# Performance work log

Hardware: AMD Instinct MI355X
Metric: run time of the kernel (lower is better)

The kernel has to match this reference:

```python
import jax, jax.numpy as jnp
import numpy as np

N = 50000      # nodes
E = 1600000    # edges (avg degree 32)
DIN, DH, DOUT = 256, 128, 64


def gcn_conv(x, W, b, row, col, w, n):
    """One GCNConv layer (self-loops already appended to row/col/w).
    row = source nodes, col = target nodes; aggregate at targets."""
    xw = x @ W                                        # [n, d_out]
    deg = jax.ops.segment_sum(w, col, num_segments=n)  # in-degree weighted
    dinv = jnp.where(deg > 0, jax.lax.rsqrt(deg), 0.0)
    norm = dinv[row] * w * dinv[col]                  # [E+n]
    msg = norm[:, None] * xw[row]                     # [E+n, d_out] gather
    out = jax.ops.segment_sum(msg, col, num_segments=n)
    return out + b


def setup_inputs() -> dict:
    key = jax.random.key(0)
    k = jax.random.split(key, 6)
    x = jax.random.normal(k[0], (N, DIN), dtype=jnp.float32)
    edge_index = jax.random.randint(k[1], (2, E), 0, N)
    edge_weight = jax.random.uniform(k[2], (E,), dtype=jnp.float32)
    W1 = jax.random.normal(k[3], (DIN, DH), dtype=jnp.float32) * (1.0 / np.sqrt(DIN))
    b1 = jnp.zeros((DH,), dtype=jnp.float32)
    W2 = jax.random.normal(k[4], (DH, DOUT), dtype=jnp.float32) * (1.0 / np.sqrt(DH))
    b2 = jnp.zeros((DOUT,), dtype=jnp.float32)
    return {"x": x, "edge_index": edge_index, "edge_weight": edge_weight,
            "W1": W1, "b1": b1, "W2": W2, "b2": b2}


def reference(x, edge_index, edge_weight, W1, b1, W2, b2):
    n = x.shape[0]
    loops = jnp.arange(n, dtype=edge_index.dtype)
    row = jnp.concatenate([edge_index[0], loops])
    col = jnp.concatenate([edge_index[1], loops])
    w = jnp.concatenate([edge_weight, jnp.ones((n,), dtype=edge_weight.dtype)])
    h = gcn_conv(x, W1, b1, row, col, w, n)
    h = jax.nn.relu(h)
    # dropout(p=0.2) is identity in eval mode
    h = gcn_conv(h, W2, b2, row, col, w, n)
    return jax.nn.log_softmax(h, axis=-1)
```

## Files before the change

### kernel.cpp

```cpp
#include <hip/hip_runtime.h>
#include <hip/hip_bf16.h>
#include <cstddef>


#define DIN 256
#define DH  128
#define DOUT 64
#define NPB 100
#define NBMAX 512

typedef __bf16 bf16x8 __attribute__((ext_vector_type(8)));
typedef float f32x4 __attribute__((ext_vector_type(4)));

__device__ __forceinline__ float bflo(unsigned u) { return __uint_as_float(u << 16); }
__device__ __forceinline__ float bfhi(unsigned u) { return __uint_as_float(u & 0xffff0000u); }
__device__ __forceinline__ unsigned short f2bf(float f) {
    unsigned u = __float_as_uint(f);
    unsigned r = (u + 0x7fffu + ((u >> 16) & 1u)) >> 16;
    return (unsigned short)r;
}

__global__ void prep_w_kernel(const float* __restrict__ W1, const float* __restrict__ W2,
                              unsigned short* __restrict__ wt1, unsigned short* __restrict__ wt2) {
    int i = blockIdx.x * 256 + threadIdx.x;
    if (i < DH * DIN) {
        int nn = i >> 8, k = i & 255;
        wt1[i] = f2bf(W1[k * DH + nn]);
    } else {
        int j = i - DH * DIN;
        if (j < DOUT * DH) {
            int nn = j >> 7, k = j & 127;
            wt2[j] = f2bf(W2[k * DOUT + nn]);
        }
    }
}

__launch_bounds__(256)
__global__ void hist_kernel(const int* __restrict__ col, int* __restrict__ bh,
                            int E, int Ec, int NB) {
    __shared__ int hist[NBMAX];
    int p = blockIdx.x, t = threadIdx.x;
    for (int b = t; b < NB; b += 256) hist[b] = 0;
    __syncthreads();
    int s = p * Ec, e = min(s + Ec, E);
    for (int i = s + t; i < e; i += 256) atomicAdd(&hist[col[i] / NPB], 1);
    __syncthreads();
    for (int b = t; b < NB; b += 256) bh[p * NB + b] = hist[b];
}

__launch_bounds__(512)
__global__ void colscan_kernel(int* __restrict__ bh, int* __restrict__ btotal,
                               int P, int NB) {
    __shared__ int arr[512];
    int b = blockIdx.x, t = threadIdx.x;
    arr[t] = (t < P) ? bh[t * NB + b] : 0;
    __syncthreads();
    for (int off = 1; off < 512; off <<= 1) {
        int v = (t >= off) ? arr[t - off] : 0;
        __syncthreads();
        arr[t] += v;
        __syncthreads();
    }
    int excl = (t == 0) ? 0 : arr[t - 1];
    if (t < P) bh[t * NB + b] = excl;
    if (t == P - 1) btotal[b] = arr[t];
}

__launch_bounds__(512)
__global__ void basescan_kernel(const int* __restrict__ btotal, int* __restrict__ bbase,
                                int* __restrict__ rowptr, int NB, int n, int E) {
    __shared__ int arr[512];
    int t = threadIdx.x;
    arr[t] = (t < NB) ? btotal[t] : 0;
    __syncthreads();
    for (int off = 1; off < 512; off <<= 1) {
        int v = (t >= off) ? arr[t - off] : 0;
        __syncthreads();
        arr[t] += v;
        __syncthreads();
    }
    int excl = (t == 0) ? 0 : arr[t - 1];
    if (t <= NB) bbase[t] = excl;
    if (t == 511) rowptr[n] = E;
}

__launch_bounds__(256)
__global__ void scatter_kernel(const int* __restrict__ row, const int* __restrict__ col,
                               const float* __restrict__ w, const int* __restrict__ bh,
                               const int* __restrict__ bbase, int2* __restrict__ part,
                               int E, int Ec, int NB) {
    __shared__ int cur[NBMAX];
    int p = blockIdx.x, t = threadIdx.x;
    for (int b = t; b < NB; b += 256) cur[b] = bbase[b] + bh[p * NB + b];
    __syncthreads();
    int s = p * Ec, e = min(s + Ec, E);
    for (int i = s + t; i < e; i += 256) {
        int c = col[i];
        int r = row[i];
        int b = c / NPB;
        int pos = atomicAdd(&cur[b], 1);
        part[pos] = make_int2(r | ((c - b * NPB) << 16), __float_as_int(w[i]));
    }
}

__launch_bounds__(256)
__global__ void bucket_csr_kernel(const int2* __restrict__ part, const int* __restrict__ bbase,
                                  float* __restrict__ dinv, int* __restrict__ rowptr,
                                  int2* __restrict__ final_e, int n) {
    __shared__ int   hist[NPB];
    __shared__ float wsum[NPB];
    __shared__ int   nbase[NPB];
    __shared__ int   cur[NPB];
    int b = blockIdx.x, t = threadIdx.x;
    if (t < NPB) { hist[t] = 0; wsum[t] = 0.0f; }
    __syncthreads();
    int s = bbase[b], e = bbase[b + 1];
    for (int i = s + t; i < e; i += 256) {
        int2 rec = part[i];
        int cl = rec.x >> 16;
        atomicAdd(&hist[cl], 1);
        atomicAdd(&wsum[cl], __int_as_float(rec.y));
    }
    __syncthreads();
    if (t == 0) {
        int run = 0;
        for (int k = 0; k < NPB; ++k) { nbase[k] = run; run += hist[k]; }
    }
    __syncthreads();
    if (t < NPB) {
        int node = b * NPB + t;
        if (node < n) {
            dinv[node] = rsqrtf(1.0f + wsum[t]);
            rowptr[node] = s + nbase[t];
        }
        cur[t] = nbase[t];
    }
    __syncthreads();
    for (int i = s + t; i < e; i += 256) {
        int2 rec = part[i];
        int cl = rec.x >> 16;
        int q = s + atomicAdd(&cur[cl], 1);
        final_e[q] = make_int2(rec.x & 0xffff, rec.y);
    }
}

template <int K, int M>
__launch_bounds__(256)
__global__ void gemm_mfma_kernel(const float* __restrict__ A,
                                 const unsigned short* __restrict__ Wt,
                                 const float* __restrict__ scale,
                                 unsigned short* __restrict__ C, int N) {
    constexpr int BK = 64, LD = BK + 8;
    constexpr int WN = M / 4;
    constexpr int NT = WN / 16;
    constexpr int CLD = M + 8;
    constexpr int SM = (64 * LD + M * LD) > (64 * CLD) ? (64 * LD + M * LD) : (64 * CLD);
    __shared__ unsigned short smem[SM];
    __shared__ float sdv[64];
    unsigned short* As = smem;
    unsigned short* Bs = smem + 64 * LD;

    const int tid = threadIdx.x;
    const int row0 = blockIdx.x * 64;
    const int lane = tid & 63;
    const int quad = lane >> 4, r16 = lane & 15;
    const int n0 = (tid >> 6) * WN;

    if (tid < 64) {
        int r = row0 + tid;
        sdv[tid] = (r < N) ? scale[r] : 0.0f;
    }

    f32x4 acc[4][NT];
#pragma unroll
    for (int mt = 0; mt < 4; ++mt)
#pragma unroll
        for (int nt = 0; nt < NT; ++nt)
            acc[mt][nt] = (f32x4){0.f, 0.f, 0.f, 0.f};

    for (int k0 = 0; k0 < K; k0 += BK) {
#pragma unroll
        for (int j = 0; j < 4; ++j) {
            int idx = tid + j * 256;
            int m = idx >> 4;
            int q = idx & 15;
            int gr = row0 + m;
            float4 v = make_float4(0.f, 0.f, 0.f, 0.f);
            if (gr < N) v = *(const float4*)&A[(size_t)gr * K + k0 + q * 4];
            ushort4 s4;
            s4.x = f2bf(v.x); s4.y = f2bf(v.y); s4.z = f2bf(v.z); s4.w = f2bf(v.w);
            *(ushort4*)&As[m * LD + q * 4] = s4;
        }
#pragma unroll
        for (int j = 0; j < M * 8 / 256; ++j) {
            int idx = tid + j * 256;
            int nn = idx >> 3;
            int q = idx & 7;
            uint4 v = *(const uint4*)&Wt[(size_t)nn * K + k0 + q * 8];
            *(uint4*)&Bs[nn * LD + q * 8] = v;
        }
        __syncthreads();
#pragma unroll
        for (int ks = 0; ks < BK / 32; ++ks) {
            bf16x8 af[4], bfr[NT];
#pragma unroll
            for (int nt = 0; nt < NT; ++nt)
                bfr[nt] = *(const bf16x8*)&Bs[(n0 + nt * 16 + r16) * LD + ks * 32 + quad * 8];
#pragma unroll
            for (int mt = 0; mt < 4; ++mt)
                af[mt] = *(const bf16x8*)&As[(mt * 16 + r16) * LD + ks * 32 + quad * 8];
#pragma unroll
            for (int mt = 0; mt < 4; ++mt)
#pragma unroll
                for (int nt = 0; nt < NT; ++nt)
                    acc[mt][nt] = __builtin_amdgcn_mfma_f32_16x16x32_bf16(
                        af[mt], bfr[nt], acc[mt][nt], 0, 0, 0);
        }
        __syncthreads();
    }
    unsigned short* Cs = smem;
#pragma unroll
    for (int mt = 0; mt < 4; ++mt) {
#pragma unroll
        for (int i = 0; i < 4; ++i) {
            int r = mt * 16 + quad * 4 + i;
            float sc = sdv[r];
#pragma unroll
            for (int nt = 0; nt < NT; ++nt)
                Cs[r * CLD + n0 + nt * 16 + r16] = f2bf(acc[mt][nt][i] * sc);
        }
    }
    __syncthreads();
#pragma unroll
    for (int j = 0; j < 64 * M / 8 / 256; ++j) {
        int idx = tid + j * 256;
        int r = idx / (M / 8);
        int q = idx % (M / 8);
        int gr = row0 + r;
        if (gr < N) {
            uint4 v = *(const uint4*)&Cs[r * CLD + q * 8];
            *(uint4*)&C[(size_t)gr * M + q * 8] = v;
        }
    }
}

__launch_bounds__(256)
__global__ void agg1_kernel(const uint2* __restrict__ xw,
                            const int* __restrict__ rowptr,
                            const int2* __restrict__ edge,
                            const float* __restrict__ dinv,
                            const float* __restrict__ bias,
                            float* __restrict__ out, int n) {
    int node = blockIdx.x * 4 + (threadIdx.x >> 6);
    if (node >= n) return;
    int lane = threadIdx.x & 63;
    int half = lane >> 5, sub = lane & 31;
    float a0 = 0.f, a1 = 0.f, a2 = 0.f, a3 = 0.f;
    if (half == 0) {
        uint2 u = xw[(size_t)node * 32 + sub];
        a0 = bflo(u.x); a1 = bfhi(u.x); a2 = bflo(u.y); a3 = bfhi(u.y);
    }
    int p = rowptr[node], p1 = rowptr[node + 1];
    for (; p + 8 <= p1; p += 8) {
        int2 e0 = edge[p + half],     e1 = edge[p + 2 + half];
        int2 e2 = edge[p + 4 + half], e3 = edge[p + 6 + half];
        uint2 v0 = xw[(size_t)e0.x * 32 + sub];
        uint2 v1 = xw[(size_t)e1.x * 32 + sub];
        uint2 v2 = xw[(size_t)e2.x * 32 + sub];
        uint2 v3 = xw[(size_t)e3.x * 32 + sub];
        float w0 = __int_as_float(e0.y), w1 = __int_as_float(e1.y);
        float w2 = __int_as_float(e2.y), w3 = __int_as_float(e3.y);
        a0 += w0 * bflo(v0.x) + w1 * bflo(v1.x) + w2 * bflo(v2.x) + w3 * bflo(v3.x);
        a1 += w0 * bfhi(v0.x) + w1 * bfhi(v1.x) + w2 * bfhi(v2.x) + w3 * bfhi(v3.x);
        a2 += w0 * bflo(v0.y) + w1 * bflo(v1.y) + w2 * bflo(v2.y) + w3 * bflo(v3.y);
        a3 += w0 * bfhi(v0.y) + w1 * bfhi(v1.y) + w2 * bfhi(v2.y) + w3 * bfhi(v3.y);
    }
    for (; p + 2 <= p1; p += 2) {
        int2 e0 = edge[p + half];
        uint2 v0 = xw[(size_t)e0.x * 32 + sub];
        float w0 = __int_as_float(e0.y);
        a0 += w0 * bflo(v0.x); a1 += w0 * bfhi(v0.x);
        a2 += w0 * bflo(v0.y); a3 += w0 * bfhi(v0.y);
    }
    if (p < p1 && half == 0) {
        int2 e0 = edge[p];
        uint2 v0 = xw[(size_t)e0.x * 32 + sub];
        float w0 = __int_as_float(e0.y);
        a0 += w0 * bflo(v0.x); a1 += w0 * bfhi(v0.x);
        a2 += w0 * bflo(v0.y); a3 += w0 * bfhi(v0.y);
    }
    a0 += __shfl_xor(a0, 32); a1 += __shfl_xor(a1, 32);
    a2 += __shfl_xor(a2, 32); a3 += __shfl_xor(a3, 32);
    float di = dinv[node];
    float4 b = ((const float4*)bias)[sub];
    a0 = fmaxf(di * a0 + b.x, 0.f);
    a1 = fmaxf(di * a1 + b.y, 0.f);
    a2 = fmaxf(di * a2 + b.z, 0.f);
    a3 = fmaxf(di * a3 + b.w, 0.f);
    if (half == 0)
        ((float4*)out)[(size_t)node * 32 + sub] = make_float4(a0, a1, a2, a3);
}

__launch_bounds__(256)
__global__ void agg2_kernel(const uint2* __restrict__ xw,
                            const int* __restrict__ rowptr,
                            const int2* __restrict__ edge,
                            const float* __restrict__ dinv,
                            const float* __restrict__ bias,
                            float* __restrict__ out, int n) {
    int node = blockIdx.x * 4 + (threadIdx.x >> 6);
    if (node >= n) return;
    int lane = threadIdx.x & 63;
    int qw = lane >> 4, sub = lane & 15;
    float a0 = 0.f, a1 = 0.f, a2 = 0.f, a3 = 0.f;
    if (qw == 0) {
        uint2 u = xw[(size_t)node * 16 + sub];
        a0 = bflo(u.x); a1 = bfhi(u.x); a2 = bflo(u.y); a3 = bfhi(u.y);
    }
    int p = rowptr[node], p1 = rowptr[node + 1];
    for (; p + 8 <= p1; p += 8) {
        int2 e0 = edge[p + qw], e1 = edge[p + 4 + qw];
        uint2 v0 = xw[(size_t)e0.x * 16 + sub];
        uint2 v1 = xw[(size_t)e1.x * 16 + sub];
        float w0 = __int_as_float(e0.y), w1 = __int_as_float(e1.y);
        a0 += w0 * bflo(v0.x) + w1 * bflo(v1.x);
        a1 += w0 * bfhi(v0.x) + w1 * bfhi(v1.x);
        a2 += w0 * bflo(v0.y) + w1 * bflo(v1.y);
        a3 += w0 * bfhi(v0.y) + w1 * bfhi(v1.y);
    }
    for (; p + 4 <= p1; p += 4) {
        int2 e0 = edge[p + qw];
        uint2 v0 = xw[(size_t)e0.x * 16 + sub];
        float w0 = __int_as_float(e0.y);
        a0 += w0 * bflo(v0.x); a1 += w0 * bfhi(v0.x);
        a2 += w0 * bflo(v0.y); a3 += w0 * bfhi(v0.y);
    }
    int rem = p1 - p;
    if (qw < rem) {
        int2 e0 = edge[p + qw];
        uint2 v0 = xw[(size_t)e0.x * 16 + sub];
        float w0 = __int_as_float(e0.y);
        a0 += w0 * bflo(v0.x); a1 += w0 * bfhi(v0.x);
        a2 += w0 * bflo(v0.y); a3 += w0 * bfhi(v0.y);
    }
    a0 += __shfl_xor(a0, 32); a1 += __shfl_xor(a1, 32);
    a2 += __shfl_xor(a2, 32); a3 += __shfl_xor(a3, 32);
    a0 += __shfl_xor(a0, 16); a1 += __shfl_xor(a1, 16);
    a2 += __shfl_xor(a2, 16); a3 += __shfl_xor(a3, 16);
    float di = dinv[node];
    float4 b = ((const float4*)bias)[sub];
    a0 = di * a0 + b.x; a1 = di * a1 + b.y;
    a2 = di * a2 + b.z; a3 = di * a3 + b.w;
    float m = fmaxf(fmaxf(a0, a1), fmaxf(a2, a3));
#pragma unroll
    for (int off = 8; off > 0; off >>= 1) m = fmaxf(m, __shfl_xor(m, off));
    float s = __expf(a0 - m) + __expf(a1 - m) + __expf(a2 - m) + __expf(a3 - m);
#pragma unroll
    for (int off = 8; off > 0; off >>= 1) s += __shfl_xor(s, off);
    float lse = m + __logf(s);
    if (qw == 0)
        ((float4*)out)[(size_t)node * 16 + sub] =
            make_float4(a0 - lse, a1 - lse, a2 - lse, a3 - lse);
}

extern "C" void kernel_launch(void* const* d_in, const int* in_sizes, int n_in,
                              void* d_out, int out_size, void* d_ws, size_t ws_size,
                              hipStream_t stream) {
    const float* x  = (const float*)d_in[0];
    const int*   ei = (const int*)d_in[1];
    const float* ew = (const float*)d_in[2];
    const float* W1 = (const float*)d_in[3];
    const float* b1 = (const float*)d_in[4];
    const float* W2 = (const float*)d_in[5];
    const float* b2 = (const float*)d_in[6];
    float* out = (float*)d_out;

    const int n = in_sizes[0] / DIN;
    const int E = in_sizes[2];
    const int* row = ei;
    const int* col = ei + E;

    const int NB = (n + NPB - 1) / NPB;
    const int P  = NB;
    const int Ec = (E + P - 1) / P;

    char* ptr = (char*)d_ws;
    auto alloc = [&](size_t bytes) -> void* {
        void* r = (void*)ptr;
        ptr += (bytes + 255) & ~(size_t)255;
        return r;
    };
    int*   bh     = (int*)  alloc((size_t)P * NB * 4);
    int*   btotal = (int*)  alloc((size_t)NB * 4);
    int*   bbase  = (int*)  alloc((size_t)(NB + 1) * 4);
    int*   rowptr = (int*)  alloc((size_t)(n + 1) * 4);
    float* dinv   = (float*)alloc((size_t)n * 4);
    int2*  edge   = (int2*) alloc((size_t)E * 8);
    unsigned short* xw1 = (unsigned short*)alloc((size_t)n * DH * 2);
    unsigned short* wt1 = (unsigned short*)alloc((size_t)DH * DIN * 2);
    unsigned short* wt2 = (unsigned short*)alloc((size_t)DOUT * DH * 2);
    char* tail = (char*)alloc((size_t)n * DH * 4);
    int2*  part = (int2*)tail;
    float* h1   = (float*)tail;
    unsigned short* xw2 = xw1;

    const int nb_g = (n + 63) / 64;
    const int nb_a = (n + 3) / 4;

    prep_w_kernel<<<(DH * DIN + DOUT * DH + 255) / 256, 256, 0, stream>>>(W1, W2, wt1, wt2);
    hist_kernel<<<P, 256, 0, stream>>>(col, bh, E, Ec, NB);
    colscan_kernel<<<NB, 512, 0, stream>>>(bh, btotal, P, NB);
    basescan_kernel<<<1, 512, 0, stream>>>(btotal, bbase, rowptr, NB, n, E);
    scatter_kernel<<<P, 256, 0, stream>>>(row, col, ew, bh, bbase, part, E, Ec, NB);
    bucket_csr_kernel<<<NB, 256, 0, stream>>>(part, bbase, dinv, rowptr, edge, n);

    gemm_mfma_kernel<DIN, DH><<<nb_g, 256, 0, stream>>>(x, wt1, dinv, xw1, n);
    agg1_kernel<<<nb_a, 256, 0, stream>>>((const uint2*)xw1, rowptr, edge, dinv, b1, h1, n);
    gemm_mfma_kernel<DH, DOUT><<<nb_g, 256, 0, stream>>>(h1, wt2, dinv, xw2, n);
    agg2_kernel<<<nb_a, 256, 0, stream>>>((const uint2*)xw2, rowptr, edge, dinv, b2, out, n);
}
```

Measured before the change: 286.6 us.

## Slice feature tables into 32-column panels and aggregate each panel separately

The GEMM outputs are now stored as column-sliced panels of 32 features (64 bytes per node), and aggregation runs one pass per panel, with each wave handling 8 edges in parallel over 8 feature lanes. The aim is to shrink the gathered working set per pass so the randomly accessed table fits in cache and the per-edge gathers hit L2 more often. The second GEMM reads the sliced h1 layout directly, and log-softmax moves into a separate kernel. In exchange the edge list is read once per panel (six passes instead of two), more kernels are launched, and the logits make an extra round trip through memory.

```diff
diff --git a/kernel.cpp b/kernel.cpp
--- a/kernel.cpp
+++ b/kernel.cpp
@@ -144,7 +144,7 @@
     }
 }
 
-template <int K, int M>
+template <int K, int M, bool ASLICED>
 __launch_bounds__(256)
 __global__ void gemm_mfma_kernel(const float* __restrict__ A,
                                  const unsigned short* __restrict__ Wt,
@@ -185,8 +185,14 @@
             int m = idx >> 4;
             int q = idx & 15;
             int gr = row0 + m;
+            int k = k0 + q * 4;
             float4 v = make_float4(0.f, 0.f, 0.f, 0.f);
-            if (gr < N) v = *(const float4*)&A[(size_t)gr * K + k0 + q * 4];
+            if (gr < N) {
+                if (ASLICED)
+                    v = *(const float4*)&A[((size_t)(k >> 5) * N + gr) * 32 + (k & 31)];
+                else
+                    v = *(const float4*)&A[(size_t)gr * K + k];
+            }
             ushort4 s4;
             s4.x = f2bf(v.x); s4.y = f2bf(v.y); s4.z = f2bf(v.z); s4.w = f2bf(v.w);
             *(ushort4*)&As[m * LD + q * 4] = s4;
@@ -239,128 +245,76 @@
         int gr = row0 + r;
         if (gr < N) {
             uint4 v = *(const uint4*)&Cs[r * CLD + q * 8];
-            *(uint4*)&C[(size_t)gr * M + q * 8] = v;
-        }
-    }
-}
-
-__launch_bounds__(256)
-__global__ void agg1_kernel(const uint2* __restrict__ xw,
-                            const int* __restrict__ rowptr,
-                            const int2* __restrict__ edge,
-                            const float* __restrict__ dinv,
-                            const float* __restrict__ bias,
-                            float* __restrict__ out, int n) {
+            *(uint4*)&C[((size_t)(q >> 2) * N + gr) * 32 + (q & 3) * 8] = v;
+        }
+    }
+}
+
+template <bool RELU>
+__launch_bounds__(256)
+__global__ void agg_pass_kernel(const unsigned short* __restrict__ tbl,
+                                const int* __restrict__ rowptr,
+                                const int2* __restrict__ edge,
+                                const float* __restrict__ dinv,
+                                const float* __restrict__ bias,
+                                float* __restrict__ outs, int n) {
+    int node = blockIdx.x * 4 + (threadIdx.x >> 6);
+    if (node >= n) return;
+    const int lane = threadIdx.x & 63;
+    const int slot = lane >> 3;
+    const int fq = lane & 7;
+    const uint2* t = (const uint2*)tbl;
+
+    float a0 = 0.f, a1 = 0.f, a2 = 0.f, a3 = 0.f;
+    if (slot == 0) {
+        uint2 u = t[(size_t)node * 8 + fq];
+        a0 = bflo(u.x); a1 = bfhi(u.x); a2 = bflo(u.y); a3 = bfhi(u.y);
+    }
+    int p0 = rowptr[node], p1 = rowptr[node + 1];
+    for (int p = p0; p < p1; p += 16) {
+        int i0 = p + slot, i1 = p + 8 + slot;
+        bool v0 = i0 < p1, v1 = i1 < p1;
+        int2 e0 = edge[v0 ? i0 : p0];
+        int2 e1 = edge[v1 ? i1 : p0];
+        float w0 = v0 ? __int_as_float(e0.y) : 0.0f;
+        float w1 = v1 ? __int_as_float(e1.y) : 0.0f;
+        uint2 g0 = t[(size_t)e0.x * 8 + fq];
+        uint2 g1 = t[(size_t)e1.x * 8 + fq];
+        a0 += w0 * bflo(g0.x) + w1 * bflo(g1.x);
+        a1 += w0 * bfhi(g0.x) + w1 * bfhi(g1.x);
+        a2 += w0 * bflo(g0.y) + w1 * bflo(g1.y);
+        a3 += w0 * bfhi(g0.y) + w1 * bfhi(g1.y);
+    }
+#pragma unroll
+    for (int off = 8; off <= 32; off <<= 1) {
+        a0 += __shfl_xor(a0, off); a1 += __shfl_xor(a1, off);
+        a2 += __shfl_xor(a2, off); a3 += __shfl_xor(a3, off);
+    }
+    float di = dinv[node];
+    float4 b = ((const float4*)bias)[fq];
+    a0 = di * a0 + b.x; a1 = di * a1 + b.y;
+    a2 = di * a2 + b.z; a3 = di * a3 + b.w;
+    if (RELU) {
+        a0 = fmaxf(a0, 0.f); a1 = fmaxf(a1, 0.f);
+        a2 = fmaxf(a2, 0.f); a3 = fmaxf(a3, 0.f);
+    }
+    if (slot == 0)
+        ((float4*)outs)[(size_t)node * 8 + fq] = make_float4(a0, a1, a2, a3);
+}
+
+__launch_bounds__(256)
+__global__ void lsm_kernel(const float* __restrict__ lg, float* __restrict__ out, int n) {
     int node = blockIdx.x * 4 + (threadIdx.x >> 6);
     if (node >= n) return;
     int lane = threadIdx.x & 63;
-    int half = lane >> 5, sub = lane & 31;
-    float a0 = 0.f, a1 = 0.f, a2 = 0.f, a3 = 0.f;
-    if (half == 0) {
-        uint2 u = xw[(size_t)node * 32 + sub];
-        a0 = bflo(u.x); a1 = bfhi(u.x); a2 = bflo(u.y); a3 = bfhi(u.y);
-    }
-    int p = rowptr[node], p1 = rowptr[node + 1];
-    for (; p + 8 <= p1; p += 8) {
-        int2 e0 = edge[p + half],     e1 = edge[p + 2 + half];
-        int2 e2 = edge[p + 4 + half], e3 = edge[p + 6 + half];
-        uint2 v0 = xw[(size_t)e0.x * 32 + sub];
-        uint2 v1 = xw[(size_t)e1.x * 32 + sub];
-        uint2 v2 = xw[(size_t)e2.x * 32 + sub];
-        uint2 v3 = xw[(size_t)e3.x * 32 + sub];
-        float w0 = __int_as_float(e0.y), w1 = __int_as_float(e1.y);
-        float w2 = __int_as_float(e2.y), w3 = __int_as_float(e3.y);
-        a0 += w0 * bflo(v0.x) + w1 * bflo(v1.x) + w2 * bflo(v2.x) + w3 * bflo(v3.x);
-        a1 += w0 * bfhi(v0.x) + w1 * bfhi(v1.x) + w2 * bfhi(v2.x) + w3 * bfhi(v3.x);
-        a2 += w0 * bflo(v0.y) + w1 * bflo(v1.y) + w2 * bflo(v2.y) + w3 * bflo(v3.y);
-        a3 += w0 * bfhi(v0.y) + w1 * bfhi(v1.y) + w2 * bfhi(v2.y) + w3 * bfhi(v3.y);
-    }
-    for (; p + 2 <= p1; p += 2) {
-        int2 e0 = edge[p + half];
-        uint2 v0 = xw[(size_t)e0.x * 32 + sub];
-        float w0 = __int_as_float(e0.y);
-        a0 += w0 * bflo(v0.x); a1 += w0 * bfhi(v0.x);
-        a2 += w0 * bflo(v0.y); a3 += w0 * bfhi(v0.y);
-    }
-    if (p < p1 && half == 0) {
-        int2 e0 = edge[p];
-        uint2 v0 = xw[(size_t)e0.x * 32 + sub];
-        float w0 = __int_as_float(e0.y);
-        a0 += w0 * bflo(v0.x); a1 += w0 * bfhi(v0.x);
-        a2 += w0 * bflo(v0.y); a3 += w0 * bfhi(v0.y);
-    }
-    a0 += __shfl_xor(a0, 32); a1 += __shfl_xor(a1, 32);
-    a2 += __shfl_xor(a2, 32); a3 += __shfl_xor(a3, 32);
-    float di = dinv[node];
-    float4 b = ((const float4*)bias)[sub];
-    a0 = fmaxf(di * a0 + b.x, 0.f);
-    a1 = fmaxf(di * a1 + b.y, 0.f);
-    a2 = fmaxf(di * a2 + b.z, 0.f);
-    a3 = fmaxf(di * a3 + b.w, 0.f);
-    if (half == 0)
-        ((float4*)out)[(size_t)node * 32 + sub] = make_float4(a0, a1, a2, a3);
-}
-
-__launch_bounds__(256)
-__global__ void agg2_kernel(const uint2* __restrict__ xw,
-                            const int* __restrict__ rowptr,
-                            const int2* __restrict__ edge,
-                            const float* __restrict__ dinv,
-                            const float* __restrict__ bias,
-                            float* __restrict__ out, int n) {
-    int node = blockIdx.x * 4 + (threadIdx.x >> 6);
-    if (node >= n) return;
-    int lane = threadIdx.x & 63;
-    int qw = lane >> 4, sub = lane & 15;
-    float a0 = 0.f, a1 = 0.f, a2 = 0.f, a3 = 0.f;
-    if (qw == 0) {
-        uint2 u = xw[(size_t)node * 16 + sub];
-        a0 = bflo(u.x); a1 = bfhi(u.x); a2 = bflo(u.y); a3 = bfhi(u.y);
-    }
-    int p = rowptr[node], p1 = rowptr[node + 1];
-    for (; p + 8 <= p1; p += 8) {
-        int2 e0 = edge[p + qw], e1 = edge[p + 4 + qw];
-        uint2 v0 = xw[(size_t)e0.x * 16 + sub];
-        uint2 v1 = xw[(size_t)e1.x * 16 + sub];
-        float w0 = __int_as_float(e0.y), w1 = __int_as_float(e1.y);
-        a0 += w0 * bflo(v0.x) + w1 * bflo(v1.x);
-        a1 += w0 * bfhi(v0.x) + w1 * bfhi(v1.x);
-        a2 += w0 * bflo(v0.y) + w1 * bflo(v1.y);
-        a3 += w0 * bfhi(v0.y) + w1 * bfhi(v1.y);
-    }
-    for (; p + 4 <= p1; p += 4) {
-        int2 e0 = edge[p + qw];
-        uint2 v0 = xw[(size_t)e0.x * 16 + sub];
-        float w0 = __int_as_float(e0.y);
-        a0 += w0 * bflo(v0.x); a1 += w0 * bfhi(v0.x);
-        a2 += w0 * bflo(v0.y); a3 += w0 * bfhi(v0.y);
-    }
-    int rem = p1 - p;
-    if (qw < rem) {
-        int2 e0 = edge[p + qw];
-        uint2 v0 = xw[(size_t)e0.x * 16 + sub];
-        float w0 = __int_as_float(e0.y);
-        a0 += w0 * bflo(v0.x); a1 += w0 * bfhi(v0.x);
-        a2 += w0 * bflo(v0.y); a3 += w0 * bfhi(v0.y);
-    }
-    a0 += __shfl_xor(a0, 32); a1 += __shfl_xor(a1, 32);
-    a2 += __shfl_xor(a2, 32); a3 += __shfl_xor(a3, 32);
-    a0 += __shfl_xor(a0, 16); a1 += __shfl_xor(a1, 16);
-    a2 += __shfl_xor(a2, 16); a3 += __shfl_xor(a3, 16);
-    float di = dinv[node];
-    float4 b = ((const float4*)bias)[sub];
-    a0 = di * a0 + b.x; a1 = di * a1 + b.y;
-    a2 = di * a2 + b.z; a3 = di * a3 + b.w;
-    float m = fmaxf(fmaxf(a0, a1), fmaxf(a2, a3));
-#pragma unroll
-    for (int off = 8; off > 0; off >>= 1) m = fmaxf(m, __shfl_xor(m, off));
-    float s = __expf(a0 - m) + __expf(a1 - m) + __expf(a2 - m) + __expf(a3 - m);
-#pragma unroll
-    for (int off = 8; off > 0; off >>= 1) s += __shfl_xor(s, off);
-    float lse = m + __logf(s);
-    if (qw == 0)
-        ((float4*)out)[(size_t)node * 16 + sub] =
-            make_float4(a0 - lse, a1 - lse, a2 - lse, a3 - lse);
+    float v = lg[((size_t)(lane >> 5) * n + node) * 32 + (lane & 31)];
+    float m = v;
+#pragma unroll
+    for (int off = 32; off > 0; off >>= 1) m = fmaxf(m, __shfl_xor(m, off));
+    float s = __expf(v - m);
+#pragma unroll
+    for (int off = 32; off > 0; off >>= 1) s += __shfl_xor(s, off);
+    out[(size_t)node * 64 + lane] = v - m - __logf(s);
 }
 
 extern "C" void kernel_launch(void* const* d_in, const int* in_sizes, int n_in,
@@ -402,6 +356,7 @@
     char* tail = (char*)alloc((size_t)n * DH * 4);
     int2*  part = (int2*)tail;
     float* h1   = (float*)tail;
+    float* lg   = (float*)tail;
     unsigned short* xw2 = xw1;
 
     const int nb_g = (n + 63) / 64;
@@ -414,8 +369,15 @@
     scatter_kernel<<<P, 256, 0, stream>>>(row, col, ew, bh, bbase, part, E, Ec, NB);
     bucket_csr_kernel<<<NB, 256, 0, stream>>>(part, bbase, dinv, rowptr, edge, n);
 
-    gemm_mfma_kernel<DIN, DH><<<nb_g, 256, 0, stream>>>(x, wt1, dinv, xw1, n);
-    agg1_kernel<<<nb_a, 256, 0, stream>>>((const uint2*)xw1, rowptr, edge, dinv, b1, h1, n);
-    gemm_mfma_kernel<DH, DOUT><<<nb_g, 256, 0, stream>>>(h1, wt2, dinv, xw2, n);
-    agg2_kernel<<<nb_a, 256, 0, stream>>>((const uint2*)xw2, rowptr, edge, dinv, b2, out, n);
-}
+    gemm_mfma_kernel<DIN, DH, false><<<nb_g, 256, 0, stream>>>(x, wt1, dinv, xw1, n);
+    for (int s = 0; s < 4; ++s)
+        agg_pass_kernel<true><<<nb_a, 256, 0, stream>>>(
+            xw1 + (size_t)s * n * 32, rowptr, edge, dinv, b1 + 32 * s,
+            h1 + (size_t)s * n * 32, n);
+    gemm_mfma_kernel<DH, DOUT, true><<<nb_g, 256, 0, stream>>>(h1, wt2, dinv, xw2, n);
+    for (int s = 0; s < 2; ++s)
+        agg_pass_kernel<false><<<nb_a, 256, 0, stream>>>(
+            xw2 + (size_t)s * n * 32, rowptr, edge, dinv, b2 + 32 * s,
+            lg + (size_t)s * n * 32, n);
+    lsm_kernel<<<nb_a, 256, 0, stream>>>(lg, out, n);
+}
```

Measured after the change: 354.4 us. +23.6%, slower.

## Overlap edge scatter with first GEMM and fold source norm into edge weights

Applied to the files above, without the earlier changes.

The first GEMM no longer depends on dinv, because the source-side normalization is folded into the edge weights by a new normw pass. That lets the GEMM share one launch with the edge scatter, the two running as different block ranges. The partition count is reduced to a fixed 128 blocks, which shrinks the histogram and column-scan work. Nontemporal loads and stores are added for streaming edge and output traffic. The cost is an extra pass over the edge list, and the scatter blocks compete with the GEMM blocks for compute units.

```diff
diff --git a/kernel.cpp b/kernel.cpp
--- a/kernel.cpp
+++ b/kernel.cpp
@@ -8,9 +8,11 @@
 #define DOUT 64
 #define NPB 100
 #define NBMAX 512
+#define PBLK 128
 
 typedef __bf16 bf16x8 __attribute__((ext_vector_type(8)));
 typedef float f32x4 __attribute__((ext_vector_type(4)));
+typedef int i32x2 __attribute__((ext_vector_type(2)));
 
 __device__ __forceinline__ float bflo(unsigned u) { return __uint_as_float(u << 16); }
 __device__ __forceinline__ float bfhi(unsigned u) { return __uint_as_float(u & 0xffff0000u); }
@@ -18,6 +20,14 @@
     unsigned u = __float_as_uint(f);
     unsigned r = (u + 0x7fffu + ((u >> 16) & 1u)) >> 16;
     return (unsigned short)r;
+}
+__device__ __forceinline__ int2 ldnt2(const int2* p) {
+    i32x2 v = __builtin_nontemporal_load((const i32x2*)p);
+    int2 r; r.x = v.x; r.y = v.y; return r;
+}
+__device__ __forceinline__ void stnt4(float* p, float a, float b, float c, float d) {
+    f32x4 v = {a, b, c, d};
+    __builtin_nontemporal_store(v, (f32x4*)p);
 }
 
 __global__ void prep_w_kernel(const float* __restrict__ W1, const float* __restrict__ W2,
@@ -43,27 +53,27 @@
     for (int b = t; b < NB; b += 256) hist[b] = 0;
     __syncthreads();
     int s = p * Ec, e = min(s + Ec, E);
-    for (int i = s + t; i < e; i += 256) atomicAdd(&hist[col[i] / NPB], 1);
+    for (int i = s + t; i < e; i += 256)
+        atomicAdd(&hist[__builtin_nontemporal_load(&col[i]) / NPB], 1);
     __syncthreads();
     for (int b = t; b < NB; b += 256) bh[p * NB + b] = hist[b];
 }
 
-__launch_bounds__(512)
-__global__ void colscan_kernel(int* __restrict__ bh, int* __restrict__ btotal,
-                               int P, int NB) {
-    __shared__ int arr[512];
+__launch_bounds__(PBLK)
+__global__ void colscan_kernel(int* __restrict__ bh, int* __restrict__ btotal, int NB) {
+    __shared__ int arr[PBLK];
     int b = blockIdx.x, t = threadIdx.x;
-    arr[t] = (t < P) ? bh[t * NB + b] : 0;
-    __syncthreads();
-    for (int off = 1; off < 512; off <<= 1) {
-        int v = (t >= off) ? arr[t - off] : 0;
-        __syncthreads();
-        arr[t] += v;
-        __syncthreads();
-    }
-    int excl = (t == 0) ? 0 : arr[t - 1];
-    if (t < P) bh[t * NB + b] = excl;
-    if (t == P - 1) btotal[b] = arr[t];
+    int v = bh[t * NB + b];
+    arr[t] = v;
+    __syncthreads();
+    for (int off = 1; off < PBLK; off <<= 1) {
+        int u = (t >= off) ? arr[t - off] : 0;
+        __syncthreads();
+        arr[t] += u;
+        __syncthreads();
+    }
+    bh[t * NB + b] = arr[t] - v;
+    if (t == PBLK - 1) btotal[b] = arr[t];
 }
 
 __launch_bounds__(512)
@@ -84,98 +94,25 @@
     if (t == 511) rowptr[n] = E;
 }
 
-__launch_bounds__(256)
-__global__ void scatter_kernel(const int* __restrict__ row, const int* __restrict__ col,
-                               const float* __restrict__ w, const int* __restrict__ bh,
-                               const int* __restrict__ bbase, int2* __restrict__ part,
-                               int E, int Ec, int NB) {
-    __shared__ int cur[NBMAX];
-    int p = blockIdx.x, t = threadIdx.x;
-    for (int b = t; b < NB; b += 256) cur[b] = bbase[b] + bh[p * NB + b];
-    __syncthreads();
-    int s = p * Ec, e = min(s + Ec, E);
-    for (int i = s + t; i < e; i += 256) {
-        int c = col[i];
-        int r = row[i];
-        int b = c / NPB;
-        int pos = atomicAdd(&cur[b], 1);
-        part[pos] = make_int2(r | ((c - b * NPB) << 16), __float_as_int(w[i]));
-    }
-}
-
-__launch_bounds__(256)
-__global__ void bucket_csr_kernel(const int2* __restrict__ part, const int* __restrict__ bbase,
-                                  float* __restrict__ dinv, int* __restrict__ rowptr,
-                                  int2* __restrict__ final_e, int n) {
-    __shared__ int   hist[NPB];
-    __shared__ float wsum[NPB];
-    __shared__ int   nbase[NPB];
-    __shared__ int   cur[NPB];
-    int b = blockIdx.x, t = threadIdx.x;
-    if (t < NPB) { hist[t] = 0; wsum[t] = 0.0f; }
-    __syncthreads();
-    int s = bbase[b], e = bbase[b + 1];
-    for (int i = s + t; i < e; i += 256) {
-        int2 rec = part[i];
-        int cl = rec.x >> 16;
-        atomicAdd(&hist[cl], 1);
-        atomicAdd(&wsum[cl], __int_as_float(rec.y));
-    }
-    __syncthreads();
-    if (t == 0) {
-        int run = 0;
-        for (int k = 0; k < NPB; ++k) { nbase[k] = run; run += hist[k]; }
-    }
-    __syncthreads();
-    if (t < NPB) {
-        int node = b * NPB + t;
-        if (node < n) {
-            dinv[node] = rsqrtf(1.0f + wsum[t]);
-            rowptr[node] = s + nbase[t];
-        }
-        cur[t] = nbase[t];
-    }
-    __syncthreads();
-    for (int i = s + t; i < e; i += 256) {
-        int2 rec = part[i];
-        int cl = rec.x >> 16;
-        int q = s + atomicAdd(&cur[cl], 1);
-        final_e[q] = make_int2(rec.x & 0xffff, rec.y);
-    }
-}
-
 template <int K, int M>
-__launch_bounds__(256)
-__global__ void gemm_mfma_kernel(const float* __restrict__ A,
-                                 const unsigned short* __restrict__ Wt,
-                                 const float* __restrict__ scale,
-                                 unsigned short* __restrict__ C, int N) {
+__device__ __forceinline__ void gemm_body(const float* __restrict__ A,
+                                          const unsigned short* __restrict__ Wt,
+                                          unsigned short* __restrict__ C,
+                                          int N, int bid, int tid, char* sraw) {
     constexpr int BK = 64, LD = BK + 8;
-    constexpr int WN = M / 4;
-    constexpr int NT = WN / 16;
-    constexpr int CLD = M + 8;
-    constexpr int SM = (64 * LD + M * LD) > (64 * CLD) ? (64 * LD + M * LD) : (64 * CLD);
-    __shared__ unsigned short smem[SM];
-    __shared__ float sdv[64];
-    unsigned short* As = smem;
-    unsigned short* Bs = smem + 64 * LD;
-
-    const int tid = threadIdx.x;
-    const int row0 = blockIdx.x * 64;
+    constexpr int WN = M / 4, NTL = WN / 16, CLD = M + 8;
+    unsigned short* As = (unsigned short*)sraw;
+    unsigned short* Bs = As + 64 * LD;
+    const int row0 = bid * 64;
     const int lane = tid & 63;
     const int quad = lane >> 4, r16 = lane & 15;
     const int n0 = (tid >> 6) * WN;
 
-    if (tid < 64) {
-        int r = row0 + tid;
-        sdv[tid] = (r < N) ? scale[r] : 0.0f;
-    }
-
-    f32x4 acc[4][NT];
+    f32x4 acc[4][NTL];
 #pragma unroll
     for (int mt = 0; mt < 4; ++mt)
 #pragma unroll
-        for (int nt = 0; nt < NT; ++nt)
+        for (int nt = 0; nt < NTL; ++nt)
             acc[mt][nt] = (f32x4){0.f, 0.f, 0.f, 0.f};
 
     for (int k0 = 0; k0 < K; k0 += BK) {
@@ -202,9 +139,9 @@
         __syncthreads();
 #pragma unroll
         for (int ks = 0; ks < BK / 32; ++ks) {
-            bf16x8 af[4], bfr[NT];
-#pragma unroll
-            for (int nt = 0; nt < NT; ++nt)
+            bf16x8 af[4], bfr[NTL];
+#pragma unroll
+            for (int nt = 0; nt < NTL; ++nt)
                 bfr[nt] = *(const bf16x8*)&Bs[(n0 + nt * 16 + r16) * LD + ks * 32 + quad * 8];
 #pragma unroll
             for (int mt = 0; mt < 4; ++mt)
@@ -212,24 +149,22 @@
 #pragma unroll
             for (int mt = 0; mt < 4; ++mt)
 #pragma unroll
-                for (int nt = 0; nt < NT; ++nt)
+                for (int nt = 0; nt < NTL; ++nt)
                     acc[mt][nt] = __builtin_amdgcn_mfma_f32_16x16x32_bf16(
                         af[mt], bfr[nt], acc[mt][nt], 0, 0, 0);
         }
         __syncthreads();
     }
-    unsigned short* Cs = smem;
-#pragma unroll
-    for (int mt = 0; mt < 4; ++mt) {
+    unsigned short* Cs = (unsigned short*)sraw;
+#pragma unroll
+    for (int mt = 0; mt < 4; ++mt)
 #pragma unroll
         for (int i = 0; i < 4; ++i) {
             int r = mt * 16 + quad * 4 + i;
-            float sc = sdv[r];
-#pragma unroll
-            for (int nt = 0; nt < NT; ++nt)
-                Cs[r * CLD + n0 + nt * 16 + r16] = f2bf(acc[mt][nt][i] * sc);
-        }
-    }
+#pragma unroll
+            for (int nt = 0; nt < NTL; ++nt)
+                Cs[r * CLD + n0 + nt * 16 + r16] = f2bf(acc[mt][nt][i]);
+        }
     __syncthreads();
 #pragma unroll
     for (int j = 0; j < 64 * M / 8 / 256; ++j) {
@@ -241,6 +176,97 @@
             uint4 v = *(const uint4*)&Cs[r * CLD + q * 8];
             *(uint4*)&C[(size_t)gr * M + q * 8] = v;
         }
+    }
+}
+
+template <int K, int M>
+__launch_bounds__(256)
+__global__ void gemm_scatter_kernel(const float* __restrict__ A,
+                                    const unsigned short* __restrict__ Wt,
+                                    unsigned short* __restrict__ C, int N,
+                                    const int* __restrict__ row, const int* __restrict__ col,
+                                    const float* __restrict__ w, const int* __restrict__ bh,
+                                    const int* __restrict__ bbase, int2* __restrict__ part,
+                                    int E, int Ec, int NB) {
+    __shared__ char sraw[(64 + M) * (64 + 8) * 2];
+    int tid = threadIdx.x;
+    if ((int)blockIdx.x < PBLK) {
+        int* cur = (int*)sraw;
+        int p = blockIdx.x;
+        for (int b = tid; b < NB; b += 256) cur[b] = bbase[b] + bh[p * NB + b];
+        __syncthreads();
+        int s = p * Ec, e = min(s + Ec, E);
+        for (int i = s + tid; i < e; i += 256) {
+            int c = __builtin_nontemporal_load(&col[i]);
+            int r = __builtin_nontemporal_load(&row[i]);
+            float wv = __builtin_nontemporal_load(&w[i]);
+            int b = c / NPB;
+            int pos = atomicAdd(&cur[b], 1);
+            i32x2 rec; rec.x = r | ((c - b * NPB) << 16); rec.y = __float_as_int(wv);
+            __builtin_nontemporal_store(rec, (i32x2*)&part[pos]);
+        }
+    } else {
+        gemm_body<K, M>(A, Wt, C, N, blockIdx.x - PBLK, tid, sraw);
+    }
+}
+
+template <int K, int M>
+__launch_bounds__(256)
+__global__ void gemm_kernel(const float* __restrict__ A, const unsigned short* __restrict__ Wt,
+                            unsigned short* __restrict__ C, int N) {
+    __shared__ char sraw[(64 + M) * (64 + 8) * 2];
+    gemm_body<K, M>(A, Wt, C, N, blockIdx.x, threadIdx.x, sraw);
+}
+
+__launch_bounds__(256)
+__global__ void bucket_csr_kernel(const int2* __restrict__ part, const int* __restrict__ bbase,
+                                  float* __restrict__ dinv, int* __restrict__ rowptr,
+                                  int2* __restrict__ final_e, int n) {
+    __shared__ int   hist[NPB];
+    __shared__ float wsum[NPB];
+    __shared__ int   nbase[NPB];
+    __shared__ int   cur[NPB];
+    int b = blockIdx.x, t = threadIdx.x;
+    if (t < NPB) { hist[t] = 0; wsum[t] = 0.0f; }
+    __syncthreads();
+    int s = bbase[b], e = bbase[b + 1];
+    for (int i = s + t; i < e; i += 256) {
+        int2 rec = part[i];
+        int cl = rec.x >> 16;
+        atomicAdd(&hist[cl], 1);
+        atomicAdd(&wsum[cl], __int_as_float(rec.y));
+    }
+    __syncthreads();
+    if (t == 0) {
+        int run = 0;
+        for (int k = 0; k < NPB; ++k) { nbase[k] = run; run += hist[k]; }
+    }
+    __syncthreads();
+    if (t < NPB) {
+        int node = b * NPB + t;
+        if (node < n) {
+            dinv[node] = rsqrtf(1.0f + wsum[t]);
+            rowptr[node] = s + nbase[t];
+        }
+        cur[t] = nbase[t];
+    }
+    __syncthreads();
+    for (int i = s + t; i < e; i += 256) {
+        int2 rec = part[i];
+        int cl = rec.x >> 16;
+        int q = s + atomicAdd(&cur[cl], 1);
+        i32x2 rec2; rec2.x = rec.x & 0xffff; rec2.y = rec.y;
+        __builtin_nontemporal_store(rec2, (i32x2*)&final_e[q]);
+    }
+}
+
+__launch_bounds__(256)
+__global__ void normw_kernel(int2* __restrict__ e, const float* __restrict__ dinv, int E) {
+    int i = blockIdx.x * 256 + threadIdx.x;
+    if (i < E) {
+        int2 r = ldnt2(&e[i]);
+        i32x2 o; o.x = r.x; o.y = __float_as_int(__int_as_float(r.y) * dinv[r.x]);
+        __builtin_nontemporal_store(o, (i32x2*)&e[i]);
     }
 }
 
@@ -255,15 +281,17 @@
     if (node >= n) return;
     int lane = threadIdx.x & 63;
     int half = lane >> 5, sub = lane & 31;
+    float di = dinv[node];
     float a0 = 0.f, a1 = 0.f, a2 = 0.f, a3 = 0.f;
     if (half == 0) {
         uint2 u = xw[(size_t)node * 32 + sub];
-        a0 = bflo(u.x); a1 = bfhi(u.x); a2 = bflo(u.y); a3 = bfhi(u.y);
+        a0 = di * bflo(u.x); a1 = di * bfhi(u.x);
+        a2 = di * bflo(u.y); a3 = di * bfhi(u.y);
     }
     int p = rowptr[node], p1 = rowptr[node + 1];
     for (; p + 8 <= p1; p += 8) {
-        int2 e0 = edge[p + half],     e1 = edge[p + 2 + half];
-        int2 e2 = edge[p + 4 + half], e3 = edge[p + 6 + half];
+        int2 e0 = ldnt2(&edge[p + half]),     e1 = ldnt2(&edge[p + 2 + half]);
+        int2 e2 = ldnt2(&edge[p + 4 + half]), e3 = ldnt2(&edge[p + 6 + half]);
         uint2 v0 = xw[(size_t)e0.x * 32 + sub];
         uint2 v1 = xw[(size_t)e1.x * 32 + sub];
         uint2 v2 = xw[(size_t)e2.x * 32 + sub];
@@ -276,14 +304,14 @@
         a3 += w0 * bfhi(v0.y) + w1 * bfhi(v1.y) + w2 * bfhi(v2.y) + w3 * bfhi(v3.y);
     }
     for (; p + 2 <= p1; p += 2) {
-        int2 e0 = edge[p + half];
+        int2 e0 = ldnt2(&edge[p + half]);
         uint2 v0 = xw[(size_t)e0.x * 32 + sub];
         float w0 = __int_as_float(e0.y);
         a0 += w0 * bflo(v0.x); a1 += w0 * bfhi(v0.x);
         a2 += w0 * bflo(v0.y); a3 += w0 * bfhi(v0.y);
     }
     if (p < p1 && half == 0) {
-        int2 e0 = edge[p];
+        int2 e0 = ldnt2(&edge[p]);
         uint2 v0 = xw[(size_t)e0.x * 32 + sub];
         float w0 = __int_as_float(e0.y);
         a0 += w0 * bflo(v0.x); a1 += w0 * bfhi(v0.x);
@@ -291,14 +319,13 @@
     }
     a0 += __shfl_xor(a0, 32); a1 += __shfl_xor(a1, 32);
     a2 += __shfl_xor(a2, 32); a3 += __shfl_xor(a3, 32);
-    float di = dinv[node];
     float4 b = ((const float4*)bias)[sub];
     a0 = fmaxf(di * a0 + b.x, 0.f);
     a1 = fmaxf(di * a1 + b.y, 0.f);
     a2 = fmaxf(di * a2 + b.z, 0.f);
     a3 = fmaxf(di * a3 + b.w, 0.f);
     if (half == 0)
-        ((float4*)out)[(size_t)node * 32 + sub] = make_float4(a0, a1, a2, a3);
+        stnt4(&out[(size_t)node * 128 + sub * 4], a0, a1, a2, a3);
 }
 
 __launch_bounds__(256)
@@ -312,14 +339,16 @@
     if (node >= n) return;
     int lane = threadIdx.x & 63;
     int qw = lane >> 4, sub = lane & 15;
+    float di = dinv[node];
     float a0 = 0.f, a1 = 0.f, a2 = 0.f, a3 = 0.f;
     if (qw == 0) {
         uint2 u = xw[(size_t)node * 16 + sub];
-        a0 = bflo(u.x); a1 = bfhi(u.x); a2 = bflo(u.y); a3 = bfhi(u.y);
+        a0 = di * bflo(u.x); a1 = di * bfhi(u.x);
+        a2 = di * bflo(u.y); a3 = di * bfhi(u.y);
     }
     int p = rowptr[node], p1 = rowptr[node + 1];
     for (; p + 8 <= p1; p += 8) {
-        int2 e0 = edge[p + qw], e1 = edge[p + 4 + qw];
+        int2 e0 = ldnt2(&edge[p + qw]), e1 = ldnt2(&edge[p + 4 + qw]);
         uint2 v0 = xw[(size_t)e0.x * 16 + sub];
         uint2 v1 = xw[(size_t)e1.x * 16 + sub];
         float w0 = __int_as_float(e0.y), w1 = __int_as_float(e1.y);
@@ -329,7 +358,7 @@
         a3 += w0 * bfhi(v0.y) + w1 * bfhi(v1.y);
     }
     for (; p + 4 <= p1; p += 4) {
-        int2 e0 = edge[p + qw];
+        int2 e0 = ldnt2(&edge[p + qw]);
         uint2 v0 = xw[(size_t)e0.x * 16 + sub];
         float w0 = __int_as_float(e0.y);
         a0 += w0 * bflo(v0.x); a1 += w0 * bfhi(v0.x);
@@ -337,7 +366,7 @@
     }
     int rem = p1 - p;
     if (qw < rem) {
-        int2 e0 = edge[p + qw];
+        int2 e0 = ldnt2(&edge[p + qw]);
         uint2 v0 = xw[(size_t)e0.x * 16 + sub];
         float w0 = __int_as_float(e0.y);
         a0 += w0 * bflo(v0.x); a1 += w0 * bfhi(v0.x);
@@ -347,7 +376,6 @@
     a2 += __shfl_xor(a2, 32); a3 += __shfl_xor(a3, 32);
     a0 += __shfl_xor(a0, 16); a1 += __shfl_xor(a1, 16);
     a2 += __shfl_xor(a2, 16); a3 += __shfl_xor(a3, 16);
-    float di = dinv[node];
     float4 b = ((const float4*)bias)[sub];
     a0 = di * a0 + b.x; a1 = di * a1 + b.y;
     a2 = di * a2 + b.z; a3 = di * a3 + b.w;
@@ -359,8 +387,7 @@
     for (int off = 8; off > 0; off >>= 1) s += __shfl_xor(s, off);
     float lse = m + __logf(s);
     if (qw == 0)
-        ((float4*)out)[(size_t)node * 16 + sub] =
-            make_float4(a0 - lse, a1 - lse, a2 - lse, a3 - lse);
+        stnt4(&out[(size_t)node * 64 + sub * 4], a0 - lse, a1 - lse, a2 - lse, a3 - lse);
 }
 
 extern "C" void kernel_launch(void* const* d_in, const int* in_sizes, int n_in,
@@ -381,8 +408,7 @@
     const int* col = ei + E;
 
     const int NB = (n + NPB - 1) / NPB;
-    const int P  = NB;
-    const int Ec = (E + P - 1) / P;
+    const int Ec = (E + PBLK - 1) / PBLK;
 
     char* ptr = (char*)d_ws;
     auto alloc = [&](size_t bytes) -> void* {
@@ -390,7 +416,7 @@
         ptr += (bytes + 255) & ~(size_t)255;
         return r;
     };
-    int*   bh     = (int*)  alloc((size_t)P * NB * 4);
+    int*   bh     = (int*)  alloc((size_t)PBLK * NB * 4);
     int*   btotal = (int*)  alloc((size_t)NB * 4);
     int*   bbase  = (int*)  alloc((size_t)(NB + 1) * 4);
     int*   rowptr = (int*)  alloc((size_t)(n + 1) * 4);
@@ -406,16 +432,17 @@
 
     const int nb_g = (n + 63) / 64;
     const int nb_a = (n + 3) / 4;
+    const int nb_e = (E + 255) / 256;
 
     prep_w_kernel<<<(DH * DIN + DOUT * DH + 255) / 256, 256, 0, stream>>>(W1, W2, wt1, wt2);
-    hist_kernel<<<P, 256, 0, stream>>>(col, bh, E, Ec, NB);
-    colscan_kernel<<<NB, 512, 0, stream>>>(bh, btotal, P, NB);
+    hist_kernel<<<PBLK, 256, 0, stream>>>(col, bh, E, Ec, NB);
+    colscan_kernel<<<NB, PBLK, 0, stream>>>(bh, btotal, NB);
     basescan_kernel<<<1, 512, 0, stream>>>(btotal, bbase, rowptr, NB, n, E);
-    scatter_kernel<<<P, 256, 0, stream>>>(row, col, ew, bh, bbase, part, E, Ec, NB);
+    gemm_scatter_kernel<DIN, DH><<<PBLK + nb_g, 256, 0, stream>>>(
+        x, wt1, xw1, n, row, col, ew, bh, bbase, part, E, Ec, NB);
     bucket_csr_kernel<<<NB, 256, 0, stream>>>(part, bbase, dinv, rowptr, edge, n);
-
-    gemm_mfma_kernel<DIN, DH><<<nb_g, 256, 0, stream>>>(x, wt1, dinv, xw1, n);
+    normw_kernel<<<nb_e, 256, 0, stream>>>(edge, dinv, E);
     agg1_kernel<<<nb_a, 256, 0, stream>>>((const uint2*)xw1, rowptr, edge, dinv, b1, h1, n);
-    gemm_mfma_kernel<DH, DOUT><<<nb_g, 256, 0, stream>>>(h1, wt2, dinv, xw2, n);
+    gemm_kernel<DH, DOUT><<<nb_g, 256, 0, stream>>>(h1, wt2, xw2, n);
     agg2_kernel<<<nb_a, 256, 0, stream>>>((const uint2*)xw2, rowptr, edge, dinv, b2, out, n);
 }
```

New measurement: 376.1 us. +31.2%, slower.
